# Optimization experiments

Hardware: AMD Instinct MI355X
Metric: run time of the kernel (lower is better)

Reference implementation:

```python
import jax, jax.numpy as jnp
import numpy as np

SHIFT = 1  # module's random shift_direction, fixed to +1 for determinism
B, C, H, W_SP = 1024, 512, 7, 7


def setup_inputs() -> dict:
    key = jax.random.key(0)
    k1, k2 = jax.random.split(key)
    x = jax.random.normal(k1, (B, C, H, W_SP), dtype=jnp.float32)
    W = jax.random.normal(k2, (256, 3, 3, 512), dtype=jnp.float32)
    return {"x": x, "W": W}


def _forward(x, W):
    # unfold along H with kernel (3,1), padding (1,0):
    # patches[b,c,kh,h,w] = x_padded[b,c,h+kh,w]
    xp = jnp.pad(x, ((0, 0), (0, 0), (1, 1), (0, 0)))
    t2 = jnp.stack([xp[:, :, k:k + H, :] for k in range(3)], axis=2)  # (B,512,3,7,7)
    # split channels 512 -> (2,256), move group dim next to H
    t2 = t2.reshape(B, 2, 256, 3, H, W_SP)
    t2 = t2.transpose(0, 2, 3, 4, 1, 5)          # (B,256,3,7,2,7)
    t2 = t2.reshape(B, 256, 3, 14, W_SP)         # interleave (h,group) -> 14
    t2 = jnp.roll(t2, SHIFT, axis=3)             # shift along interleaved dim
    t2 = t2.reshape(B, 256, 3, 7, 2, W_SP).sum(axis=4)  # (B,256,3,7,7)
    t2 = t2.transpose(0, 1, 3, 2, 4)             # (B,256,7,3,7) = (m,l,n,j,w)
    # second shift + unfold along w with kernel 3, padding 1
    t3 = jnp.roll(t2, SHIFT, axis=4)
    tp = jnp.pad(t3, ((0, 0), (0, 0), (0, 0), (0, 0), (1, 1)))
    t3u = jnp.stack([tp[..., k:k + W_SP] for k in range(3)], axis=4)  # (B,256,7,3,3,7) = (m,l,n,j,k,p)
    # torch einsum 'mlnjok, ljki -> mnoi' with o = output position, k = kernel tap
    out = jnp.einsum('mlnjkp,ljki->mpni', t3u, W)  # wait: check axis order below
    # Note: torch permutes (m,c,h,j,kernel,pos)->(m,c,h,j,pos,kernel) before einsum,
    # so contraction is over (l,j,kernel) and output is (m, n=h, o=pos, i).
    out = jnp.einsum('mlnjkp,ljki->mnpi', t3u, W)  # (B,7,7,512)
    return out.transpose(0, 3, 1, 2)              # (B,512,7,7)


def reference(x, W):
    return _forward(x, W)
```

## Files before the change

kernel.cpp:

```cpp
#include <hip/hip_runtime.h>
#include <hip/hip_bf16.h>


typedef __bf16 bf16x8 __attribute__((ext_vector_type(8)));
typedef float f32x4 __attribute__((ext_vector_type(4)));
typedef unsigned int u32;

#define VT_OFFSET (4u << 20)
#define VT_BYTES  (7168ull * 7 * 768 * 2)
#define WS_NEED   (VT_OFFSET + VT_BYTES)

__device__ __forceinline__ void gload_lds16(const void* g, void* l) {
    __builtin_amdgcn_global_load_lds(
        (const __attribute__((address_space(1))) u32*)g,
        (__attribute__((address_space(3))) u32*)l, 16, 0, 0);
}

__global__ __launch_bounds__(256) void prep_w(const float* __restrict__ Wg,
                                              __bf16* __restrict__ W2) {
    __shared__ float ws_[96][65];
    const int kt = blockIdx.x % 24;
    const int it_ = blockIdx.x / 24;
    const int K0 = kt * 96;
    const int I0 = it_ * 64;
    const int tid = threadIdx.x;

    #pragma unroll
    for (int t = 0; t < 6; ++t) {
        const int u = t * 256 + tid;
        const int row = u >> 4;
        const int f4 = u & 15;
        const float4 v = *(const float4*)(Wg + (size_t)(K0 + row) * 512 + I0 + f4 * 4);
        ws_[row][f4 * 4 + 0] = v.x;
        ws_[row][f4 * 4 + 1] = v.y;
        ws_[row][f4 * 4 + 2] = v.z;
        ws_[row][f4 * 4 + 3] = v.w;
    }
    __syncthreads();

    #pragma unroll
    for (int t = 0; t < 3; ++t) {
        const int u = t * 256 + tid;
        const int i = u / 12;
        const int rem = u - i * 12;
        const int tap = rem >> 2;
        const int q = rem & 3;
        bf16x8 o;
        #pragma unroll
        for (int e = 0; e < 8; ++e) {
            const int c_loc = q * 8 + e;
            o[e] = (__bf16)ws_[3 * c_loc + tap][i];
        }
        *(bf16x8*)(W2 + (size_t)(I0 + i) * 2304 + tap * 768 + 32 * kt + q * 8) = o;
    }
}

__global__ __launch_bounds__(256) void prep_v(const float* __restrict__ x,
                                              __bf16* __restrict__ Vt) {
    __shared__ float xs[256 * 49];
    const int b = blockIdx.x >> 1;
    const int g = blockIdx.x & 1;
    const int tid = threadIdx.x;

    {
        const float4* src0 = (const float4*)(x + ((size_t)b * 512 + g * 128) * 49);
        const float4* src1 = (const float4*)(x + ((size_t)b * 512 + 256 + g * 128) * 49);
        float4* dst0 = (float4*)xs;
        float4* dst1 = (float4*)(xs + 128 * 49);
        #pragma unroll
        for (int it = 0; it < 7; ++it) {
            const int q = it * 256 + tid;
            if (q < 1568) dst0[q] = src0[q];
        }
        #pragma unroll
        for (int it = 0; it < 7; ++it) {
            const int q = it * 256 + tid;
            if (q < 1568) dst1[q] = src1[q];
        }
    }
    __syncthreads();

    for (int h = 0; h < 7; ++h) {
        const int hm = (h + 6) % 7;
        for (int it = 0; it < 2; ++it) {
            const int u = it * 256 + tid;
            if (u < 336) {
                const int r = u / 48;
                const int k = u - r * 48;
                const int w = (r + 6) % 7;
                bf16x8 vv;
                #pragma unroll
                for (int e = 0; e < 8; ++e) {
                    const int c = k * 8 + e;
                    const int l = c / 3;
                    const int j = c - 3 * l;
                    const int r1 = h + j - 1;
                    const int r2 = hm + j - 1;
                    float v = 0.f;
                    if (r1 >= 0 && r1 < 7) v += xs[l * 49 + r1 * 7 + w];
                    if (r2 >= 0 && r2 < 7) v += xs[(128 + l) * 49 + r2 * 7 + w];
                    vv[e] = (__bf16)v;
                }
                *(bf16x8*)(Vt + (size_t)((b * 7 + h) * 7 + r) * 768 + g * 384 + k * 8) = vv;
            }
        }
    }
}

__global__ __launch_bounds__(256) void gemm_vt(const __bf16* __restrict__ Vt,
                                               const __bf16* __restrict__ W2,
                                               float* __restrict__ out) {
    __shared__ __align__(1024) char L[64640];

    const int tid = threadIdx.x;
    const int g0 = blockIdx.x;
    const int nb = (g0 >> 3) & 3;
    const int mb = ((g0 >> 5) << 3) | (g0 & 7);
    const int i0 = nb * 128;

    if (tid < 32) {
        const int off = (tid < 16) ? 7168 + tid * 4 : 14400 + (tid - 16) * 4;
        *(int*)(L + off) = 0;
    }

    int tsrc[2];
    #pragma unroll
    for (int it = 0; it < 2; ++it) {
        const int u = it * 256 + tid;
        if (u < 448) {
            const int bh = u / 28;
            const int rem = u - bh * 28;
            const int ct = rem >> 2;
            const int qs = rem & 3;
            const int q = qs ^ (ct & 3);
            tsrc[it] = ((mb * 16 + bh) * 7 + ct) * 1536 + q * 16;
        } else {
            tsrc[it] = 0;
        }
    }
    int bsrc[6];
    #pragma unroll
    for (int it = 0; it < 6; ++it) {
        const int s = it * 256 + tid;
        const int tap = s >> 9;
        const int rem = s & 511;
        const int n = rem >> 2;
        const int qs = rem & 3;
        const int q = qs ^ ((n >> 1) & 3);
        bsrc[it] = ((i0 + n) * 2304 + tap * 768 + q * 8) * 2;
    }

    const int lane = tid & 63;
    const int wave = tid >> 6;
    const int wm = wave >> 1;
    const int wn = wave & 1;
    const int ln15 = lane & 15;
    const int gq = lane >> 4;

    int afoff[3][4], bfoff[3][4];
    #pragma unroll
    for (int tap = 0; tap < 3; ++tap) {
        #pragma unroll
        for (int mf = 0; mf < 4; ++mf) {
            const int bh_l = wm * 8 + mf * 2 + (ln15 >> 3);
            const int p = ln15 & 7;
            const int ct = p + tap - 1;
            afoff[tap][mf] = (ct >= 0 && ct <= 6)
                ? bh_l * 448 + ct * 64 + ((gq ^ (ct & 3)) * 16)
                : 7168;
        }
        #pragma unroll
        for (int nf = 0; nf < 4; ++nf) {
            const int n_l = wn * 64 + nf * 16 + ln15;
            bfoff[tap][nf] = tap * 8192 + n_l * 64 + ((gq ^ ((n_l >> 1) & 3)) * 16);
        }
    }

    f32x4 acc[4][4];
    #pragma unroll
    for (int a = 0; a < 4; ++a)
        #pragma unroll
        for (int bq = 0; bq < 4; ++bq) acc[a][bq] = (f32x4){0.f, 0.f, 0.f, 0.f};

    const char* VtB = (const char*)Vt;
    const char* W2B = (const char*)W2;

    auto stage = [&](int ck, int buf) {
        const char* vb = VtB + ck * 64;
        char* td = L + buf * 7232;
        gload_lds16(vb + tsrc[0], td + tid * 16);
        if (tid < 192)
            gload_lds16(vb + tsrc[1], td + 4096 + tid * 16);
        else
            gload_lds16(VtB, L + 63616 + (tid - 192) * 16);
        const char* wb = W2B + ck * 64;
        char* bd = L + 14464 + buf * 24576;
        #pragma unroll
        for (int it = 0; it < 6; ++it)
            gload_lds16(wb + bsrc[it], bd + it * 4096 + tid * 16);
    };

    stage(0, 0);
    stage(1, 1);
    asm volatile("s_waitcnt lgkmcnt(0)" ::: "memory");

    for (int chunk = 0; chunk < 24; ++chunk) {
        const int cur = chunk & 1;

        if (chunk < 23) asm volatile("s_waitcnt vmcnt(8)" ::: "memory");
        else            asm volatile("s_waitcnt vmcnt(0)" ::: "memory");
        __builtin_amdgcn_s_barrier();

        const char* Tb = L + cur * 7232;
        const char* Bb = L + 14464 + cur * 24576;

        bf16x8 af[3][4], bfr[3][4];
        #pragma unroll
        for (int tap = 0; tap < 3; ++tap) {
            #pragma unroll
            for (int mf = 0; mf < 4; ++mf)
                af[tap][mf] = *(const bf16x8*)(Tb + afoff[tap][mf]);
            #pragma unroll
            for (int nf = 0; nf < 4; ++nf)
                bfr[tap][nf] = *(const bf16x8*)(Bb + bfoff[tap][nf]);
        }
        asm volatile("s_waitcnt lgkmcnt(0)" ::: "memory");
        __builtin_amdgcn_sched_barrier(0);
        __builtin_amdgcn_s_barrier();

        if (chunk + 2 < 24) stage(chunk + 2, cur);

        #pragma unroll
        for (int tap = 0; tap < 3; ++tap)
            #pragma unroll
            for (int mf = 0; mf < 4; ++mf)
                #pragma unroll
                for (int nf = 0; nf < 4; ++nf)
                    acc[mf][nf] = __builtin_amdgcn_mfma_f32_16x16x32_bf16(
                        af[tap][mf], bfr[tap][nf], acc[mf][nf], 0, 0, 0);
    }

    #pragma unroll
    for (int mf = 0; mf < 4; ++mf) {
        #pragma unroll
        for (int r = 0; r < 4; ++r) {
            const int mrow = gq * 4 + r;
            const int Mg_l = wm * 64 + mf * 16 + mrow;
            const int p = Mg_l & 7;
            if (p == 7) continue;
            const int bh_l = Mg_l >> 3;
            const int bhg = mb * 16 + bh_l;
            const int b = bhg / 7;
            const int h = bhg - 7 * b;
            #pragma unroll
            for (int nf = 0; nf < 4; ++nf) {
                const int i = i0 + wn * 64 + nf * 16 + ln15;
                out[(((size_t)b * 512 + i) * 7 + h) * 7 + p] = acc[mf][nf][r];
            }
        }
    }
}

__global__ __launch_bounds__(256) void gemm_shift(const float* __restrict__ x,
                                                  const __bf16* __restrict__ W2,
                                                  float* __restrict__ out) {
    __shared__ __bf16 T[16 * 10 * 40];
    __shared__ __bf16 Bt[128 * 104];

    const int tid = threadIdx.x;
    const int mb = blockIdx.x >> 2;
    const int nb = blockIdx.x & 3;
    const int i0 = nb * 128;

    const int cl  = tid & 31;
    const int bh0 = tid >> 5;
    const int bhg0 = mb * 16 + bh0;
    const int bhg1 = bhg0 + 8;
    const int b0 = bhg0 / 7, h0 = bhg0 - 7 * b0;
    const int b1 = bhg1 / 7, h1 = bhg1 - 7 * b1;
    const int hm0 = (h0 + 6) % 7, hm1 = (h1 + 6) % 7;

    for (int q = tid; q < 16 * 10 * 40 / 2; q += 256) ((int*)T)[q] = 0;

    const int lane = tid & 63;
    const int wave = tid >> 6;
    const int wm = wave >> 1;
    const int wn = wave & 1;
    const int ln15 = lane & 15;
    const int gq = lane >> 4;

    f32x4 acc[4][4];
    #pragma unroll
    for (int a = 0; a < 4; ++a)
        #pragma unroll
        for (int bq = 0; bq < 4; ++bq) acc[a][bq] = (f32x4){0.f, 0.f, 0.f, 0.f};

    __syncthreads();

    for (int chunk = 0; chunk < 24; ++chunk) {
        const int cg = chunk * 32 + cl;
        const int l = cg / 3;
        const int j = cg - 3 * l;
        {
            const int r1 = h0 + j - 1, r2 = hm0 + j - 1;
            float v[7] = {0.f, 0.f, 0.f, 0.f, 0.f, 0.f, 0.f};
            if (r1 >= 0 && r1 < 7) {
                const float* p1 = x + (((size_t)b0 * 512 + l) * 7 + r1) * 7;
                #pragma unroll
                for (int w = 0; w < 7; ++w) v[w] += p1[w];
            }
            if (r2 >= 0 && r2 < 7) {
                const float* p2 = x + (((size_t)b0 * 512 + 256 + l) * 7 + r2) * 7;
                #pragma unroll
                for (int w = 0; w < 7; ++w) v[w] += p2[w];
            }
            #pragma unroll
            for (int w = 0; w < 7; ++w)
                T[bh0 * 400 + ((w + 1) % 7 + 1) * 40 + cl] = (__bf16)v[w];
        }
        {
            const int r1 = h1 + j - 1, r2 = hm1 + j - 1;
            float v[7] = {0.f, 0.f, 0.f, 0.f, 0.f, 0.f, 0.f};
            if (r1 >= 0 && r1 < 7) {
                const float* p1 = x + (((size_t)b1 * 512 + l) * 7 + r1) * 7;
                #pragma unroll
                for (int w = 0; w < 7; ++w) v[w] += p1[w];
            }
            if (r2 >= 0 && r2 < 7) {
                const float* p2 = x + (((size_t)b1 * 512 + 256 + l) * 7 + r2) * 7;
                #pragma unroll
                for (int w = 0; w < 7; ++w) v[w] += p2[w];
            }
            #pragma unroll
            for (int w = 0; w < 7; ++w)
                T[(bh0 + 8) * 400 + ((w + 1) % 7 + 1) * 40 + cl] = (__bf16)v[w];
        }

        #pragma unroll
        for (int it = 0; it < 6; ++it) {
            const int u = it * 256 + tid;
            const int tap = u >> 9;
            const int rem = u & 511;
            const int n = rem >> 2;
            const int q = rem & 3;
            const float4 val = *(const float4*)(W2 + (size_t)(i0 + n) * 2304 +
                                                tap * 768 + chunk * 32 + q * 8);
            *(float4*)(&Bt[n * 104 + tap * 32 + q * 8]) = val;
        }

        __syncthreads();

        #pragma unroll
        for (int tap = 0; tap < 3; ++tap) {
            bf16x8 af[4], bfr[4];
            #pragma unroll
            for (int mf = 0; mf < 4; ++mf) {
                const int bh_l = wm * 8 + mf * 2 + (ln15 >> 3);
                const int p = ln15 & 7;
                af[mf] = *(const bf16x8*)(&T[(bh_l * 10 + p + tap) * 40 + gq * 8]);
            }
            #pragma unroll
            for (int nf = 0; nf < 4; ++nf) {
                const int n_l = wn * 64 + nf * 16 + ln15;
                bfr[nf] = *(const bf16x8*)(&Bt[n_l * 104 + tap * 32 + gq * 8]);
            }
            #pragma unroll
            for (int mf = 0; mf < 4; ++mf)
                #pragma unroll
                for (int nf = 0; nf < 4; ++nf)
                    acc[mf][nf] = __builtin_amdgcn_mfma_f32_16x16x32_bf16(
                        af[mf], bfr[nf], acc[mf][nf], 0, 0, 0);
        }

        __syncthreads();
    }

    #pragma unroll
    for (int mf = 0; mf < 4; ++mf) {
        #pragma unroll
        for (int r = 0; r < 4; ++r) {
            const int mrow = gq * 4 + r;
            const int Mg_l = wm * 64 + mf * 16 + mrow;
            const int p = Mg_l & 7;
            if (p == 7) continue;
            const int bh_l = Mg_l >> 3;
            const int bhg = mb * 16 + bh_l;
            const int b = bhg / 7;
            const int h = bhg - 7 * b;
            #pragma unroll
            for (int nf = 0; nf < 4; ++nf) {
                const int i = i0 + wn * 64 + nf * 16 + ln15;
                out[(((size_t)b * 512 + i) * 7 + h) * 7 + p] = acc[mf][nf][r];
            }
        }
    }
}

extern "C" void kernel_launch(void* const* d_in, const int* in_sizes, int n_in,
                              void* d_out, int out_size, void* d_ws, size_t ws_size,
                              hipStream_t stream) {
    const float* x  = (const float*)d_in[0];
    const float* Wg = (const float*)d_in[1];
    float* out = (float*)d_out;
    __bf16* W2 = (__bf16*)d_ws;

    prep_w<<<dim3(192), dim3(256), 0, stream>>>(Wg, W2);

    if (ws_size >= WS_NEED) {
        __bf16* Vt = (__bf16*)((char*)d_ws + VT_OFFSET);
        prep_v<<<dim3(2048), dim3(256), 0, stream>>>(x, Vt);
        gemm_vt<<<dim3(448 * 4), dim3(256), 0, stream>>>(Vt, W2, out);
    } else {
        gemm_shift<<<dim3(448 * 4), dim3(256), 0, stream>>>(x, W2, out);
    }
}
```

Before: 360.5 us.

## Double gemm_vt M tile to 256 rows and interleave LDS reads with MFMAs

The gemm_vt kernel now computes a 256-row by 128-column output tile per block (32 b·h rows instead of 16). Each wave holds an 8x4 accumulator array, and the grid is halved to 896 blocks. The goal is to reuse each staged W2 tile across twice as many rows, which cuts global and LDS traffic for B per output. The main loop now reads fragments per tap right before their MFMAs and only issues the next stage after compute. That trades some load/compute overlap and higher register and LDS use (80 KB, launch bounds 2) for fewer blocks and less redundant staging.

```diff
diff --git a/kernel.cpp b/kernel.cpp
--- a/kernel.cpp
+++ b/kernel.cpp
@@ -107,10 +107,10 @@
     }
 }
 
-__global__ __launch_bounds__(256) void gemm_vt(const __bf16* __restrict__ Vt,
-                                               const __bf16* __restrict__ W2,
-                                               float* __restrict__ out) {
-    __shared__ __align__(1024) char L[64640];
+__global__ __launch_bounds__(256, 2) void gemm_vt(const __bf16* __restrict__ Vt,
+                                                  const __bf16* __restrict__ W2,
+                                                  float* __restrict__ out) {
+    __shared__ __align__(1024) char L[80000];
 
     const int tid = threadIdx.x;
     const int g0 = blockIdx.x;
@@ -119,23 +119,33 @@
     const int i0 = nb * 128;
 
     if (tid < 32) {
-        const int off = (tid < 16) ? 7168 + tid * 4 : 14400 + (tid - 16) * 4;
+        const int off = (tid < 16) ? 14336 + tid * 4 : 28736 + (tid - 16) * 4;
         *(int*)(L + off) = 0;
     }
 
-    int tsrc[2];
-    #pragma unroll
-    for (int it = 0; it < 2; ++it) {
-        const int u = it * 256 + tid;
-        if (u < 448) {
-            const int bh = u / 28;
-            const int rem = u - bh * 28;
-            const int ct = rem >> 2;
-            const int qs = rem & 3;
-            const int q = qs ^ (ct & 3);
-            tsrc[it] = ((mb * 16 + bh) * 7 + ct) * 1536 + q * 16;
-        } else {
-            tsrc[it] = 0;
+    const int lane = tid & 63;
+    const int wave = tid >> 6;
+
+    int tsrc[4], tdoff[4], tdadd[4];
+    {
+        const int u0 = tid + wave * 192;
+        #pragma unroll
+        for (int k = 0; k < 4; ++k) {
+            const int u = u0 + k * 64;
+            if (u < 896) {
+                const int bh = u / 28;
+                const int rem = u - bh * 28;
+                const int ct = rem >> 2;
+                const int qs = rem & 3;
+                const int q = qs ^ (ct & 3);
+                tsrc[k] = ((mb * 32 + bh) * 7 + ct) * 1536 + q * 16;
+                tdoff[k] = u * 16;
+                tdadd[k] = 14400;
+            } else {
+                tsrc[k] = lane * 16;
+                tdoff[k] = 77952 + (u - 896) * 16;
+                tdadd[k] = 0;
+            }
         }
     }
     int bsrc[6];
@@ -150,6 +160,130 @@
         bsrc[it] = ((i0 + n) * 2304 + tap * 768 + q * 8) * 2;
     }
 
+    const int wm = wave >> 1;
+    const int wn = wave & 1;
+    const int ln15 = lane & 15;
+    const int gq = lane >> 4;
+
+    int afoff[3][8], bfoff[3][4];
+    #pragma unroll
+    for (int tap = 0; tap < 3; ++tap) {
+        #pragma unroll
+        for (int mf = 0; mf < 8; ++mf) {
+            const int bh_l = wm * 16 + mf * 2 + (ln15 >> 3);
+            const int p = ln15 & 7;
+            const int ct = p + tap - 1;
+            afoff[tap][mf] = (ct >= 0 && ct <= 6)
+                ? bh_l * 448 + ct * 64 + ((gq ^ (ct & 3)) * 16)
+                : 14336;
+        }
+        #pragma unroll
+        for (int nf = 0; nf < 4; ++nf) {
+            const int n_l = wn * 64 + nf * 16 + ln15;
+            bfoff[tap][nf] = tap * 8192 + n_l * 64 + ((gq ^ ((n_l >> 1) & 3)) * 16);
+        }
+    }
+
+    f32x4 acc[8][4];
+    #pragma unroll
+    for (int a = 0; a < 8; ++a)
+        #pragma unroll
+        for (int bq = 0; bq < 4; ++bq) acc[a][bq] = (f32x4){0.f, 0.f, 0.f, 0.f};
+
+    const char* VtB = (const char*)Vt;
+    const char* W2B = (const char*)W2;
+
+    auto stage = [&](int ck, int buf) {
+        const char* vb = VtB + ck * 64;
+        #pragma unroll
+        for (int k = 0; k < 4; ++k)
+            gload_lds16(vb + tsrc[k], L + tdoff[k] + buf * tdadd[k]);
+        const char* wb = W2B + ck * 64;
+        char* bd = L + 28800 + buf * 24576;
+        #pragma unroll
+        for (int it = 0; it < 6; ++it)
+            gload_lds16(wb + bsrc[it], bd + it * 4096 + tid * 16);
+    };
+
+    stage(0, 0);
+    stage(1, 1);
+    asm volatile("s_waitcnt lgkmcnt(0)" ::: "memory");
+
+    for (int chunk = 0; chunk < 24; ++chunk) {
+        const int cur = chunk & 1;
+
+        if (chunk < 23) asm volatile("s_waitcnt vmcnt(10)" ::: "memory");
+        else            asm volatile("s_waitcnt vmcnt(0)" ::: "memory");
+        __builtin_amdgcn_s_barrier();
+
+        const char* Tb = L + cur * 14400;
+        const char* Bb = L + 28800 + cur * 24576;
+
+        #pragma unroll
+        for (int tap = 0; tap < 3; ++tap) {
+            bf16x8 af[8], bfr[4];
+            #pragma unroll
+            for (int mf = 0; mf < 8; ++mf)
+                af[mf] = *(const bf16x8*)(Tb + afoff[tap][mf]);
+            #pragma unroll
+            for (int nf = 0; nf < 4; ++nf)
+                bfr[nf] = *(const bf16x8*)(Bb + bfoff[tap][nf]);
+            #pragma unroll
+            for (int mf = 0; mf < 8; ++mf)
+                #pragma unroll
+                for (int nf = 0; nf < 4; ++nf)
+                    acc[mf][nf] = __builtin_amdgcn_mfma_f32_16x16x32_bf16(
+                        af[mf], bfr[nf], acc[mf][nf], 0, 0, 0);
+        }
+
+        asm volatile("s_waitcnt lgkmcnt(0)" ::: "memory");
+        __builtin_amdgcn_sched_barrier(0);
+        __builtin_amdgcn_s_barrier();
+        if (chunk + 2 < 24) stage(chunk + 2, cur);
+    }
+
+    #pragma unroll
+    for (int mf = 0; mf < 8; ++mf) {
+        #pragma unroll
+        for (int r = 0; r < 4; ++r) {
+            const int mrow = gq * 4 + r;
+            const int Mg_l = wm * 128 + mf * 16 + mrow;
+            const int p = Mg_l & 7;
+            if (p == 7) continue;
+            const int bh_l = Mg_l >> 3;
+            const int bhg = mb * 32 + bh_l;
+            const int b = bhg / 7;
+            const int h = bhg - 7 * b;
+            #pragma unroll
+            for (int nf = 0; nf < 4; ++nf) {
+                const int i = i0 + wn * 64 + nf * 16 + ln15;
+                out[(((size_t)b * 512 + i) * 7 + h) * 7 + p] = acc[mf][nf][r];
+            }
+        }
+    }
+}
+
+__global__ __launch_bounds__(256) void gemm_shift(const float* __restrict__ x,
+                                                  const __bf16* __restrict__ W2,
+                                                  float* __restrict__ out) {
+    __shared__ __bf16 T[16 * 10 * 40];
+    __shared__ __bf16 Bt[128 * 104];
+
+    const int tid = threadIdx.x;
+    const int mb = blockIdx.x >> 2;
+    const int nb = blockIdx.x & 3;
+    const int i0 = nb * 128;
+
+    const int cl  = tid & 31;
+    const int bh0 = tid >> 5;
+    const int bhg0 = mb * 16 + bh0;
+    const int bhg1 = bhg0 + 8;
+    const int b0 = bhg0 / 7, h0 = bhg0 - 7 * b0;
+    const int b1 = bhg1 / 7, h1 = bhg1 - 7 * b1;
+    const int hm0 = (h0 + 6) % 7, hm1 = (h1 + 6) % 7;
+
+    for (int q = tid; q < 16 * 10 * 40 / 2; q += 256) ((int*)T)[q] = 0;
+
     const int lane = tid & 63;
     const int wave = tid >> 6;
     const int wm = wave >> 1;
@@ -157,87 +291,90 @@
     const int ln15 = lane & 15;
     const int gq = lane >> 4;
 
-    int afoff[3][4], bfoff[3][4];
-    #pragma unroll
-    for (int tap = 0; tap < 3; ++tap) {
-        #pragma unroll
-        for (int mf = 0; mf < 4; ++mf) {
-            const int bh_l = wm * 8 + mf * 2 + (ln15 >> 3);
-            const int p = ln15 & 7;
-            const int ct = p + tap - 1;
-            afoff[tap][mf] = (ct >= 0 && ct <= 6)
-                ? bh_l * 448 + ct * 64 + ((gq ^ (ct & 3)) * 16)
-                : 7168;
-        }
-        #pragma unroll
-        for (int nf = 0; nf < 4; ++nf) {
-            const int n_l = wn * 64 + nf * 16 + ln15;
-            bfoff[tap][nf] = tap * 8192 + n_l * 64 + ((gq ^ ((n_l >> 1) & 3)) * 16);
-        }
-    }
-
     f32x4 acc[4][4];
     #pragma unroll
     for (int a = 0; a < 4; ++a)
         #pragma unroll
         for (int bq = 0; bq < 4; ++bq) acc[a][bq] = (f32x4){0.f, 0.f, 0.f, 0.f};
 
-    const char* VtB = (const char*)Vt;
-    const char* W2B = (const char*)W2;
-
-    auto stage = [&](int ck, int buf) {
-        const char* vb = VtB + ck * 64;
-        char* td = L + buf * 7232;
-        gload_lds16(vb + tsrc[0], td + tid * 16);
-        if (tid < 192)
-            gload_lds16(vb + tsrc[1], td + 4096 + tid * 16);
-        else
-            gload_lds16(VtB, L + 63616 + (tid - 192) * 16);
-        const char* wb = W2B + ck * 64;
-        char* bd = L + 14464 + buf * 24576;
-        #pragma unroll
-        for (int it = 0; it < 6; ++it)
-            gload_lds16(wb + bsrc[it], bd + it * 4096 + tid * 16);
-    };
-
-    stage(0, 0);
-    stage(1, 1);
-    asm volatile("s_waitcnt lgkmcnt(0)" ::: "memory");
+    __syncthreads();
 
     for (int chunk = 0; chunk < 24; ++chunk) {
-        const int cur = chunk & 1;
-
-        if (chunk < 23) asm volatile("s_waitcnt vmcnt(8)" ::: "memory");
-        else            asm volatile("s_waitcnt vmcnt(0)" ::: "memory");
-        __builtin_amdgcn_s_barrier();
-
-        const char* Tb = L + cur * 7232;
-        const char* Bb = L + 14464 + cur * 24576;
-
-        bf16x8 af[3][4], bfr[3][4];
+        const int cg = chunk * 32 + cl;
+        const int l = cg / 3;
+        const int j = cg - 3 * l;
+        {
+            const int r1 = h0 + j - 1, r2 = hm0 + j - 1;
+            float v[7] = {0.f, 0.f, 0.f, 0.f, 0.f, 0.f, 0.f};
+            if (r1 >= 0 && r1 < 7) {
+                const float* p1 = x + (((size_t)b0 * 512 + l) * 7 + r1) * 7;
+                #pragma unroll
+                for (int w = 0; w < 7; ++w) v[w] += p1[w];
+            }
+            if (r2 >= 0 && r2 < 7) {
+                const float* p2 = x + (((size_t)b0 * 512 + 256 + l) * 7 + r2) * 7;
+                #pragma unroll
+                for (int w = 0; w < 7; ++w) v[w] += p2[w];
+            }
+            #pragma unroll
+            for (int w = 0; w < 7; ++w)
+                T[bh0 * 400 + ((w + 1) % 7 + 1) * 40 + cl] = (__bf16)v[w];
+        }
+        {
+            const int r1 = h1 + j - 1, r2 = hm1 + j - 1;
+            float v[7] = {0.f, 0.f, 0.f, 0.f, 0.f, 0.f, 0.f};
+            if (r1 >= 0 && r1 < 7) {
+                const float* p1 = x + (((size_t)b1 * 512 + l) * 7 + r1) * 7;
+                #pragma unroll
+                for (int w = 0; w < 7; ++w) v[w] += p1[w];
+            }
+            if (r2 >= 0 && r2 < 7) {
+                const float* p2 = x + (((size_t)b1 * 512 + 256 + l) * 7 + r2) * 7;
+                #pragma unroll
+                for (int w = 0; w < 7; ++w) v[w] += p2[w];
+            }
+            #pragma unroll
+            for (int w = 0; w < 7; ++w)
+                T[(bh0 + 8) * 400 + ((w + 1) % 7 + 1) * 40 + cl] = (__bf16)v[w];
+        }
+
+        #pragma unroll
+        for (int it = 0; it < 6; ++it) {
+            const int u = it * 256 + tid;
+            const int tap = u >> 9;
+            const int rem = u & 511;
+            const int n = rem >> 2;
+            const int q = rem & 3;
+            const float4 val = *(const float4*)(W2 + (size_t)(i0 + n) * 2304 +
+                                                tap * 768 + chunk * 32 + q * 8);
+            *(float4*)(&Bt[n * 104 + tap * 32 + q * 8]) = val;
+        }
+
+        __syncthreads();
+
         #pragma unroll
         for (int tap = 0; tap < 3; ++tap) {
-            #pragma unroll
-            for (int mf = 0; mf < 4; ++mf)
-                af[tap][mf] = *(const bf16x8*)(Tb + afoff[tap][mf]);
-            #pragma unroll
-            for (int nf = 0; nf < 4; ++nf)
-                bfr[tap][nf] = *(const bf16x8*)(Bb + bfoff[tap][nf]);
-        }
-        asm volatile("s_waitcnt lgkmcnt(0)" ::: "memory");
-        __builtin_amdgcn_sched_barrier(0);
-        __builtin_amdgcn_s_barrier();
-
-        if (chunk + 2 < 24) stage(chunk + 2, cur);
-
-        #pragma unroll
-        for (int tap = 0; tap < 3; ++tap)
+            bf16x8 af[4], bfr[4];
+            #pragma unroll
+            for (int mf = 0; mf < 4; ++mf) {
+                const int bh_l = wm * 8 + mf * 2 + (ln15 >> 3);
+                const int p = ln15 & 7;
+                af[mf] = *(const bf16x8*)(&T[(bh_l * 10 + p + tap) * 40 + gq * 8]);
+            }
+            #pragma unroll
+            for (int nf = 0; nf < 4; ++nf) {
+                const int n_l = wn * 64 + nf * 16 + ln15;
+                bfr[nf] = *(const bf16x8*)(&Bt[n_l * 104 + tap * 32 + gq * 8]);
+            }
             #pragma unroll
             for (int mf = 0; mf < 4; ++mf)
                 #pragma unroll
                 for (int nf = 0; nf < 4; ++nf)
                     acc[mf][nf] = __builtin_amdgcn_mfma_f32_16x16x32_bf16(
-                        af[tap][mf], bfr[tap][nf], acc[mf][nf], 0, 0, 0);
+                        af[mf], bfr[nf], acc[mf][nf], 0, 0, 0);
+        }
+
+        __syncthreads();
     }
 
     #pragma unroll
@@ -261,141 +398,6 @@
     }
 }
 
-__global__ __launch_bounds__(256) void gemm_shift(const float* __restrict__ x,
-                                                  const __bf16* __restrict__ W2,
-                                                  float* __restrict__ out) {
-    __shared__ __bf16 T[16 * 10 * 40];
-    __shared__ __bf16 Bt[128 * 104];
-
-    const int tid = threadIdx.x;
-    const int mb = blockIdx.x >> 2;
-    const int nb = blockIdx.x & 3;
-    const int i0 = nb * 128;
-
-    const int cl  = tid & 31;
-    const int bh0 = tid >> 5;
-    const int bhg0 = mb * 16 + bh0;
-    const int bhg1 = bhg0 + 8;
-    const int b0 = bhg0 / 7, h0 = bhg0 - 7 * b0;
-    const int b1 = bhg1 / 7, h1 = bhg1 - 7 * b1;
-    const int hm0 = (h0 + 6) % 7, hm1 = (h1 + 6) % 7;
-
-    for (int q = tid; q < 16 * 10 * 40 / 2; q += 256) ((int*)T)[q] = 0;
-
-    const int lane = tid & 63;
-    const int wave = tid >> 6;
-    const int wm = wave >> 1;
-    const int wn = wave & 1;
-    const int ln15 = lane & 15;
-    const int gq = lane >> 4;
-
-    f32x4 acc[4][4];
-    #pragma unroll
-    for (int a = 0; a < 4; ++a)
-        #pragma unroll
-        for (int bq = 0; bq < 4; ++bq) acc[a][bq] = (f32x4){0.f, 0.f, 0.f, 0.f};
-
-    __syncthreads();
-
-    for (int chunk = 0; chunk < 24; ++chunk) {
-        const int cg = chunk * 32 + cl;
-        const int l = cg / 3;
-        const int j = cg - 3 * l;
-        {
-            const int r1 = h0 + j - 1, r2 = hm0 + j - 1;
-            float v[7] = {0.f, 0.f, 0.f, 0.f, 0.f, 0.f, 0.f};
-            if (r1 >= 0 && r1 < 7) {
-                const float* p1 = x + (((size_t)b0 * 512 + l) * 7 + r1) * 7;
-                #pragma unroll
-                for (int w = 0; w < 7; ++w) v[w] += p1[w];
-            }
-            if (r2 >= 0 && r2 < 7) {
-                const float* p2 = x + (((size_t)b0 * 512 + 256 + l) * 7 + r2) * 7;
-                #pragma unroll
-                for (int w = 0; w < 7; ++w) v[w] += p2[w];
-            }
-            #pragma unroll
-            for (int w = 0; w < 7; ++w)
-                T[bh0 * 400 + ((w + 1) % 7 + 1) * 40 + cl] = (__bf16)v[w];
-        }
-        {
-            const int r1 = h1 + j - 1, r2 = hm1 + j - 1;
-            float v[7] = {0.f, 0.f, 0.f, 0.f, 0.f, 0.f, 0.f};
-            if (r1 >= 0 && r1 < 7) {
-                const float* p1 = x + (((size_t)b1 * 512 + l) * 7 + r1) * 7;
-                #pragma unroll
-                for (int w = 0; w < 7; ++w) v[w] += p1[w];
-            }
-            if (r2 >= 0 && r2 < 7) {
-                const float* p2 = x + (((size_t)b1 * 512 + 256 + l) * 7 + r2) * 7;
-                #pragma unroll
-                for (int w = 0; w < 7; ++w) v[w] += p2[w];
-            }
-            #pragma unroll
-            for (int w = 0; w < 7; ++w)
-                T[(bh0 + 8) * 400 + ((w + 1) % 7 + 1) * 40 + cl] = (__bf16)v[w];
-        }
-
-        #pragma unroll
-        for (int it = 0; it < 6; ++it) {
-            const int u = it * 256 + tid;
-            const int tap = u >> 9;
-            const int rem = u & 511;
-            const int n = rem >> 2;
-            const int q = rem & 3;
-            const float4 val = *(const float4*)(W2 + (size_t)(i0 + n) * 2304 +
-                                                tap * 768 + chunk * 32 + q * 8);
-            *(float4*)(&Bt[n * 104 + tap * 32 + q * 8]) = val;
-        }
-
-        __syncthreads();
-
-        #pragma unroll
-        for (int tap = 0; tap < 3; ++tap) {
-            bf16x8 af[4], bfr[4];
-            #pragma unroll
-            for (int mf = 0; mf < 4; ++mf) {
-                const int bh_l = wm * 8 + mf * 2 + (ln15 >> 3);
-                const int p = ln15 & 7;
-                af[mf] = *(const bf16x8*)(&T[(bh_l * 10 + p + tap) * 40 + gq * 8]);
-            }
-            #pragma unroll
-            for (int nf = 0; nf < 4; ++nf) {
-                const int n_l = wn * 64 + nf * 16 + ln15;
-                bfr[nf] = *(const bf16x8*)(&Bt[n_l * 104 + tap * 32 + gq * 8]);
-            }
-            #pragma unroll
-            for (int mf = 0; mf < 4; ++mf)
-                #pragma unroll
-                for (int nf = 0; nf < 4; ++nf)
-                    acc[mf][nf] = __builtin_amdgcn_mfma_f32_16x16x32_bf16(
-                        af[mf], bfr[nf], acc[mf][nf], 0, 0, 0);
-        }
-
-        __syncthreads();
-    }
-
-    #pragma unroll
-    for (int mf = 0; mf < 4; ++mf) {
-        #pragma unroll
-        for (int r = 0; r < 4; ++r) {
-            const int mrow = gq * 4 + r;
-            const int Mg_l = wm * 64 + mf * 16 + mrow;
-            const int p = Mg_l & 7;
-            if (p == 7) continue;
-            const int bh_l = Mg_l >> 3;
-            const int bhg = mb * 16 + bh_l;
-            const int b = bhg / 7;
-            const int h = bhg - 7 * b;
-            #pragma unroll
-            for (int nf = 0; nf < 4; ++nf) {
-                const int i = i0 + wn * 64 + nf * 16 + ln15;
-                out[(((size_t)b * 512 + i) * 7 + h) * 7 + p] = acc[mf][nf][r];
-            }
-        }
-    }
-}
-
 extern "C" void kernel_launch(void* const* d_in, const int* in_sizes, int n_in,
                               void* d_out, int out_size, void* d_ws, size_t ws_size,
                               hipStream_t stream) {
@@ -409,7 +411,7 @@
     if (ws_size >= WS_NEED) {
         __bf16* Vt = (__bf16*)((char*)d_ws + VT_OFFSET);
         prep_v<<<dim3(2048), dim3(256), 0, stream>>>(x, Vt);
-        gemm_vt<<<dim3(448 * 4), dim3(256), 0, stream>>>(Vt, W2, out);
+        gemm_vt<<<dim3(896), dim3(256), 0, stream>>>(Vt, W2, out);
     } else {
         gemm_shift<<<dim3(448 * 4), dim3(256), 0, stream>>>(x, W2, out);
     }
```

Result: no change. 365.3 us (+1.3%).
